# Performance work log

Measured on AMD Instinct MI355X. Metric: run time of the kernel, lower is better.

The kernel has to match this reference:

```python
import jax, jax.numpy as jnp
import numpy as np

B, S = 32, 128
VIDEO_SIZE, TITLE_SIZE = 768, 768
NUM_TAG, NUM_VOCAB, HIDDEN = 10000, 21128, 256


def setup_inputs() -> dict:
    key = jax.random.key(0)
    ks = jax.random.split(key, 10)
    video_feature = jax.random.normal(ks[0], (B, VIDEO_SIZE), dtype=jnp.float32)
    title_feature = jax.random.normal(ks[1], (B, S, TITLE_SIZE), dtype=jnp.float32)
    label_tag = jax.random.uniform(ks[2], (B, NUM_TAG), dtype=jnp.float32)
    label_mlm = jax.random.randint(ks[3], (B, S), 0, NUM_VOCAB, dtype=jnp.int64)
    Wt = jax.random.normal(ks[4], (NUM_TAG, VIDEO_SIZE), dtype=jnp.float32) * 0.02
    bt = jnp.zeros((NUM_TAG,), dtype=jnp.float32)
    Wm = jax.random.normal(ks[5], (NUM_VOCAB, TITLE_SIZE), dtype=jnp.float32) * 0.02
    bm = jnp.zeros((NUM_VOCAB,), dtype=jnp.float32)
    Wh = jax.random.normal(ks[6], (HIDDEN, VIDEO_SIZE + TITLE_SIZE), dtype=jnp.float32) * 0.02
    bh = jnp.zeros((HIDDEN,), dtype=jnp.float32)
    return {
        "video_feature": video_feature,
        "title_feature": title_feature,
        "label_tag": label_tag,
        "label_mlm": label_mlm,
        "Wt": Wt, "bt": bt, "Wm": Wm, "bm": bm, "Wh": Wh, "bh": bh,
    }


def reference(video_feature, title_feature, label_tag, label_mlm, Wt, bt, Wm, bm, Wh, bh):
    # tag head + BCEWithLogits (mean reduction), numerically stable form
    pred_tag = video_feature @ Wt.T + bt                       # [B, NUM_TAG]
    loss_tag = jnp.mean(
        jnp.maximum(pred_tag, 0.0) - pred_tag * label_tag
        + jnp.log1p(jnp.exp(-jnp.abs(pred_tag)))
    )
    pred_tag_sig = jax.nn.sigmoid(pred_tag)

    # mlm head: per-token vocab logits, masked CE summed over nonzero labels
    logits = jnp.einsum('bsd,vd->bsv', title_feature, Wm) + bm  # [B, S, V]
    lse = jax.nn.logsumexp(logits, axis=-1)                     # [B, S]
    gold = jnp.take_along_axis(logits, label_mlm[..., None], axis=-1)[..., 0]
    ce = lse - gold                                             # per-token NLL
    mask = (label_mlm != 0)
    loss_mlm = jnp.sum(jnp.where(mask, ce, 0.0))

    # fused embedding head + L2 normalize (torch eps 1e-12)
    feature = jnp.concatenate([video_feature, title_feature[:, 0]], axis=1)
    embedding = feature @ Wh.T + bh                             # [B, HIDDEN]
    norm = jnp.linalg.norm(embedding, axis=1, keepdims=True)
    normed_embedding = embedding / jnp.maximum(norm, 1e-12)

    return (pred_tag_sig, normed_embedding, loss_tag, loss_mlm)
```

## Files before the change

kernel.cpp:

```cpp
#include <hip/hip_runtime.h>
#include <hip/hip_bf16.h>
#include <math.h>

typedef short bf16x8 __attribute__((ext_vector_type(8)));
typedef float f32x4 __attribute__((ext_vector_type(4)));

#define KDIM 768
#define NTAG 10000
#define NVOC 21128
#define HID 256
#define NTOK 4096
#define NCHUNK 24
#define CHUNK 881
#define NTILE 28
#define TILEB 24576
#define M0 4.0f
#define WMSCALE 16.0f
#define INVSCALE 0.0625f
#define LOG2E 1.44269504f

#define WS_A     0ull
#define WS_AVID  3145728ull
#define WS_PSUM  3194880ull
#define WS_GOLD  3588096ull
#define WS_TAGL  3604480ull
#define WS_WM8   3604544ull
#define WS_NEED  (WS_WM8 + 16515072ull + 65536ull)

#define OUT_EMB  320000
#define OUT_LTAG 328192
#define OUT_LMLM 328193

#define MLM_BLKS 768
#define TAG_BLKS 313
#define GOLD_BLKS 256
#define EMB_BLKS 32
#define CONV_BLKS 1548
#define WMCV_BLKS (NCHUNK*NTILE)

typedef const __attribute__((address_space(1))) unsigned int glds_g;
typedef __attribute__((address_space(3))) unsigned int glds_l;

static __device__ __forceinline__ unsigned short f2bf(float f) {
  unsigned u = __builtin_bit_cast(unsigned, f);
  u = u + 0x7FFFu + ((u >> 16) & 1u);
  return (unsigned short)(u >> 16);
}

static __device__ __forceinline__ int pk4_fp8(float4 v, float scale) {
  int w = __builtin_amdgcn_cvt_pk_fp8_f32(v.x * scale, v.y * scale, 0, false);
  w = __builtin_amdgcn_cvt_pk_fp8_f32(v.z * scale, v.w * scale, w, true);
  return w;
}

static __device__ __forceinline__ bf16x8 cvt8(float4 f0, float4 f1) {
  bf16x8 o;
  o[0] = (short)f2bf(f0.x); o[1] = (short)f2bf(f0.y);
  o[2] = (short)f2bf(f0.z); o[3] = (short)f2bf(f0.w);
  o[4] = (short)f2bf(f1.x); o[5] = (short)f2bf(f1.y);
  o[6] = (short)f2bf(f1.z); o[7] = (short)f2bf(f1.w);
  return o;
}

__global__ __launch_bounds__(256) void k_conv(
    const float* __restrict__ title, const float* __restrict__ video,
    const float* __restrict__ Wm,
    char* __restrict__ A8, unsigned short* __restrict__ Avid,
    char* __restrict__ Wm8, float* __restrict__ tagSum) {
  __shared__ __align__(1024) char tsm[TILEB];
  const int bid = blockIdx.x, tid = threadIdx.x;
  if (bid < CONV_BLKS) {
    const int nT = 393216;
    int i = bid * 256 + tid;
    if (i == 0) tagSum[0] = 0.f;
    if (i < nT) {
      float4 v0 = ((const float4*)title)[i * 2];
      float4 v1 = ((const float4*)title)[i * 2 + 1];
      int2 o = {pk4_fp8(v0, 1.f), pk4_fp8(v1, 1.f)};
      *(int2*)(A8 + (size_t)i * 8) = o;
    } else {
      int j = i - nT;
      float4 v0 = ((const float4*)video)[j * 2];
      float4 v1 = ((const float4*)video)[j * 2 + 1];
      *(bf16x8*)(Avid + (size_t)j * 8) = cvt8(v0, v1);
    }
  } else {
    const int wblk = bid - CONV_BLKS;
    const int chunk = wblk / NTILE, tile = wblk % NTILE;
    const int n0 = chunk * CHUNK + tile * 32;
    const int nend = min(chunk * CHUNK + CHUNK, NVOC);
    #pragma unroll
    for (int j = 0; j < 12; ++j) {
      int p = j * 256 + tid;
      int r = p / 96, q = p % 96;
      int n = n0 + r;
      int2 o = {0, 0};
      if (n < nend) {
        const float* wp = Wm + (size_t)n * KDIM + q * 8;
        o.x = pk4_fp8(((const float4*)wp)[0], WMSCALE);
        o.y = pk4_fp8(((const float4*)wp)[1], WMSCALE);
      }
      *(int2*)(tsm + (q >> 2) * 1024 + (q & 3) * 256 + r * 8) = o;
    }
    __syncthreads();
    char* dst = Wm8 + (size_t)wblk * TILEB;
    #pragma unroll
    for (int j = 0; j < 6; ++j) {
      int idx = j * 256 + tid;
      *(int4*)(dst + idx * 16) = *(const int4*)(tsm + idx * 16);
    }
  }
}

template<bool WM8>
__global__ __launch_bounds__(256)
__attribute__((amdgpu_waves_per_eu(3, 3)))
void k_main(
    const char* __restrict__ A8,
    const float* __restrict__ Wm,
    const char* __restrict__ Wm8,
    const float* __restrict__ bm,
    float* __restrict__ psum,
    const unsigned short* __restrict__ Avid,
    const float* __restrict__ Wt, const float* __restrict__ bt,
    const float* __restrict__ ylab,
    const float* __restrict__ title, const int* __restrict__ lab,
    const float* __restrict__ video,
    const float* __restrict__ Wh, const float* __restrict__ bh,
    float* __restrict__ out_sig, float* __restrict__ tagSum,
    float* __restrict__ gold, float* __restrict__ out_emb) {
  __shared__ __align__(1024) char smem[2 * TILEB + 3584];
  const int bid = blockIdx.x, tid = threadIdx.x;
  const int wave = tid >> 6, lane = tid & 63, g = lane >> 4, col16 = lane & 15;

  if (bid < MLM_BLKS) {
    char (*Bsm)[TILEB] = (char(*)[TILEB])smem;
    float* biasS = (float*)(smem + 2 * TILEB);
    const int chunk = bid % NCHUNK, mt = bid / NCHUNK;
    const int nbeg = chunk * CHUNK;
    const int nend = min(nbeg + CHUNK, NVOC);
    const int col = col16;

    for (int i = tid; i < NTILE * 32; i += 256) {
      int n = nbeg + i;
      biasS[i] = (n < nend) ? (bm[n] - M0) * LOG2E : -1e30f;
    }

    const int arow0 = mt * 128 + wave * 32;
    long a0[24], a1[24];
    #pragma unroll
    for (int kk = 0; kk < 24; ++kk) {
      a0[kk] = *(const long*)(A8 + (size_t)(arow0 + col) * KDIM + kk * 32 + g * 8);
      a1[kk] = *(const long*)(A8 + (size_t)(arow0 + 16 + col) * KDIM + kk * 32 + g * 8);
    }

    float s[8];
    #pragma unroll
    for (int i = 0; i < 8; ++i) s[i] = 0.f;

    const int off0 = col * 8 + g * 256;
    const float kinv = INVSCALE * LOG2E;

    auto COMPUTE = [&](int t) {
      const char* B = &Bsm[t & 1][0] + off0;
      f32x4 acc00 = {0.f,0.f,0.f,0.f}, acc10 = {0.f,0.f,0.f,0.f};
      f32x4 acc01 = {0.f,0.f,0.f,0.f}, acc11 = {0.f,0.f,0.f,0.f};
      #pragma unroll
      for (int kk = 0; kk < 24; ++kk) {
        long b0 = *(const long*)(B + kk * 1024);
        long b1 = *(const long*)(B + kk * 1024 + 128);
        acc00 = __builtin_amdgcn_mfma_f32_16x16x32_fp8_fp8(a0[kk], b0, acc00, 0, 0, 0);
        acc10 = __builtin_amdgcn_mfma_f32_16x16x32_fp8_fp8(a1[kk], b0, acc10, 0, 0, 0);
        acc01 = __builtin_amdgcn_mfma_f32_16x16x32_fp8_fp8(a0[kk], b1, acc01, 0, 0, 0);
        acc11 = __builtin_amdgcn_mfma_f32_16x16x32_fp8_fp8(a1[kk], b1, acc11, 0, 0, 0);
      }
      const float b20 = biasS[t * 32 + col];
      const float b21 = biasS[t * 32 + 16 + col];
      #pragma unroll
      for (int rr = 0; rr < 4; ++rr) {
        s[rr]     += exp2f(fmaf(acc00[rr], kinv, b20)) + exp2f(fmaf(acc01[rr], kinv, b21));
        s[rr + 4] += exp2f(fmaf(acc10[rr], kinv, b20)) + exp2f(fmaf(acc11[rr], kinv, b21));
      }
    };

    if constexpr (WM8) {
      const char* cbase = Wm8 + (size_t)chunk * NTILE * TILEB;
      auto STAGE = [&](int buf, int tt) {
        const char* src = cbase + (size_t)tt * TILEB + wave * 1024 + lane * 16;
        char* dst = &Bsm[buf][0] + wave * 1024;
        #pragma unroll
        for (int j = 0; j < 6; ++j) {
          __builtin_amdgcn_global_load_lds((glds_g*)(src + j * 4096),
                                           (glds_l*)(dst + j * 4096), 16, 0, 0);
        }
      };
      STAGE(0, 0);
      asm volatile("s_waitcnt lgkmcnt(0)" ::: "memory");
      __builtin_amdgcn_s_barrier();
      for (int t = 0; t < NTILE; ++t) {
        int tn = (t + 1 < NTILE) ? t + 1 : 0;
        STAGE((t + 1) & 1, tn);
        asm volatile("s_waitcnt vmcnt(6)" ::: "memory");
        __builtin_amdgcn_s_barrier();
        __builtin_amdgcn_sched_barrier(0);
        __builtin_amdgcn_s_setprio(1);
        COMPUTE(t);
        __builtin_amdgcn_s_setprio(0);
        __builtin_amdgcn_sched_barrier(0);
        __builtin_amdgcn_s_barrier();
      }
    } else {
      __syncthreads();
      for (int t = 0; t < NTILE; ++t) {
        #pragma unroll
        for (int j = 0; j < 6; ++j) {
          int sg = j * 256 + tid;
          int kk = sg >> 6, gg = (sg >> 4) & 3, nl0 = (sg & 15) * 2;
          int n_a = nbeg + t * 32 + nl0, n_b = n_a + 1;
          int4 o = {0, 0, 0, 0};
          if (n_a < nend) {
            const float* wp = Wm + (size_t)n_a * KDIM + kk * 32 + gg * 8;
            o.x = pk4_fp8(((const float4*)wp)[0], WMSCALE);
            o.y = pk4_fp8(((const float4*)wp)[1], WMSCALE);
          }
          if (n_b < nend) {
            const float* wp = Wm + (size_t)n_b * KDIM + kk * 32 + gg * 8;
            o.z = pk4_fp8(((const float4*)wp)[0], WMSCALE);
            o.w = pk4_fp8(((const float4*)wp)[1], WMSCALE);
          }
          *(int4*)(&Bsm[0][0] + kk * 1024 + gg * 256 + nl0 * 8) = o;
        }
        __syncthreads();
        COMPUTE(t);
        __syncthreads();
      }
    }

    #pragma unroll
    for (int i = 0; i < 8; ++i) {
      float v = s[i];
      v += __shfl_xor(v, 1);
      v += __shfl_xor(v, 2);
      v += __shfl_xor(v, 4);
      v += __shfl_xor(v, 8);
      s[i] = v;
    }
    if (col == 0) {
      #pragma unroll
      for (int mblk = 0; mblk < 2; ++mblk)
        #pragma unroll
        for (int rr = 0; rr < 4; ++rr) {
          int tok = arow0 + mblk * 16 + g * 4 + rr;
          psum[tok * NCHUNK + chunk] = s[mblk * 4 + rr];
        }
    }

  } else if (bid < MLM_BLKS + TAG_BLKS) {
    const int tb = bid - MLM_BLKS;
    unsigned short* Bt = (unsigned short*)smem;
    float* wsum = (float*)(smem + 49152);
    #pragma unroll
    for (int j = 0; j < 12; ++j) {
      int sg = j * 256 + tid;
      int tt = (j >= 6) ? 1 : 0;
      int sgl = sg - tt * 1536;
      int kk = sgl >> 6, c = (sgl & 63) >> 2, gg = sgl & 3;
      int n = (tb * 2 + tt) * 16 + c;
      bf16x8 o = {};
      if (n < NTAG) {
        const float* wp = Wt + (size_t)n * KDIM + kk * 32 + gg * 8;
        o = cvt8(((const float4*)wp)[0], ((const float4*)wp)[1]);
      }
      *(bf16x8*)((char*)Bt + sg * 16) = o;
    }
    __syncthreads();

    const int ntile = tb * 2 + (wave >> 1), mhalf = wave & 1;
    float lacc = 0.f;
    if (ntile < 625) {
      bf16x8 a[24];
      #pragma unroll
      for (int kk = 0; kk < 24; ++kk)
        a[kk] = *(const bf16x8*)(Avid + (size_t)(mhalf * 16 + col16) * KDIM + kk * 32 + g * 8);
      const char* Bb = (const char*)Bt + (wave >> 1) * 24576 + col16 * 64 + g * 16;
      f32x4 acc = {0.f, 0.f, 0.f, 0.f};
      #pragma unroll
      for (int kk = 0; kk < 24; ++kk) {
        bf16x8 b = *(const bf16x8*)(Bb + kk * 1024);
        acc = __builtin_amdgcn_mfma_f32_16x16x32_bf16(a[kk], b, acc, 0, 0, 0);
      }
      const int nc = ntile * 16 + col16;
      if (nc < NTAG) {
        const float bias = bt[nc];
        #pragma unroll
        for (int rr = 0; rr < 4; ++rr) {
          int brow = mhalf * 16 + g * 4 + rr;
          float x = acc[rr] + bias;
          out_sig[(size_t)brow * NTAG + nc] = 1.f / (1.f + __expf(-x));
          float y = ylab[(size_t)brow * NTAG + nc];
          lacc += fmaxf(x, 0.f) - x * y + log1pf(__expf(-fabsf(x)));
        }
      }
    }
    #pragma unroll
    for (int m = 32; m; m >>= 1) lacc += __shfl_xor(lacc, m);
    if (lane == 0) wsum[wave] = lacc;
    __syncthreads();
    if (tid == 0) atomicAdd(tagSum, wsum[0] + wsum[1] + wsum[2] + wsum[3]);

  } else if (bid < MLM_BLKS + TAG_BLKS + GOLD_BLKS) {
    const int tbase = (bid - MLM_BLKS - TAG_BLKS) * 16;
    #pragma unroll
    for (int u = 0; u < 4; ++u) {
      int tok = tbase + wave * 4 + u;
      int l = lab[tok];
      float acc = 0.f;
      #pragma unroll
      for (int j = 0; j < 12; ++j) {
        int k = j * 64 + lane;
        acc += title[(size_t)tok * KDIM + k] * Wm[(size_t)l * KDIM + k];
      }
      #pragma unroll
      for (int m = 32; m; m >>= 1) acc += __shfl_xor(acc, m);
      if (lane == 0) gold[tok] = acc + bm[l];
    }

  } else {
    float* feat = (float*)smem;
    float* red = (float*)(smem + 49152);
    const int b = bid - MLM_BLKS - TAG_BLKS - GOLD_BLKS;
    #pragma unroll
    for (int j = 0; j < 6; ++j) {
      int k = j * 256 + tid;
      feat[k] = (k < KDIM) ? video[(size_t)b * KDIM + k]
                           : title[(size_t)b * 128 * KDIM + (k - KDIM)];
    }
    __syncthreads();
    float acc = bh[tid];
    #pragma unroll 8
    for (int k = 0; k < 1536; k += 4) {
      float4 w = *(const float4*)(Wh + (size_t)tid * 1536 + k);
      acc += w.x * feat[k] + w.y * feat[k + 1] + w.z * feat[k + 2] + w.w * feat[k + 3];
    }
    float ss = acc * acc;
    #pragma unroll
    for (int m = 32; m; m >>= 1) ss += __shfl_xor(ss, m);
    if (lane == 0) red[wave] = ss;
    __syncthreads();
    float nrm = sqrtf(red[0] + red[1] + red[2] + red[3]);
    float scale = 1.f / fmaxf(nrm, 1e-12f);
    out_emb[(size_t)b * HID + tid] = acc * scale;
  }
}

__global__ __launch_bounds__(256) void k_final(
    const float* __restrict__ psum, const float* __restrict__ gold,
    const int* __restrict__ lab, const float* __restrict__ tagSum,
    float* __restrict__ out) {
  __shared__ float red[4];
  const int tid = threadIdx.x, wave = tid >> 6, lane = tid & 63;
  if (tid == 0) out[OUT_LTAG] = tagSum[0] / 320000.f;

  float lm = 0.f;
  for (int tok = tid; tok < NTOK; tok += 256) {
    float S = 0.f;
    #pragma unroll
    for (int c = 0; c < NCHUNK; ++c) S += psum[tok * NCHUNK + c];
    float lse = M0 + logf(S);
    if (lab[tok] != 0) lm += lse - gold[tok];
  }
  #pragma unroll
  for (int m = 32; m; m >>= 1) lm += __shfl_xor(lm, m);
  if (lane == 0) red[wave] = lm;
  __syncthreads();
  if (tid == 0) out[OUT_LMLM] = red[0] + red[1] + red[2] + red[3];
}

extern "C" void kernel_launch(void* const* d_in, const int* in_sizes, int n_in,
                              void* d_out, int out_size, void* d_ws, size_t ws_size,
                              hipStream_t stream) {
  const float* video = (const float*)d_in[0];
  const float* title = (const float*)d_in[1];
  const float* ylab  = (const float*)d_in[2];
  const int*   lab   = (const int*)d_in[3];
  const float* Wt = (const float*)d_in[4];
  const float* bt = (const float*)d_in[5];
  const float* Wm = (const float*)d_in[6];
  const float* bm = (const float*)d_in[7];
  const float* Wh = (const float*)d_in[8];
  const float* bh = (const float*)d_in[9];
  float* out = (float*)d_out;
  char* ws = (char*)d_ws;

  char* wsA8   = ws + WS_A;
  unsigned short* wsAvid = (unsigned short*)(ws + WS_AVID);
  float* wsPsum = (float*)(ws + WS_PSUM);
  float* wsGold = (float*)(ws + WS_GOLD);
  float* wsTagl = (float*)(ws + WS_TAGL);
  char* wsWm8  = ws + WS_WM8;

  const bool useWm8 = ws_size >= WS_NEED;
  const int mainGrid = MLM_BLKS + TAG_BLKS + GOLD_BLKS + EMB_BLKS;

  k_conv<<<CONV_BLKS + WMCV_BLKS, 256, 0, stream>>>(
      title, video, Wm, wsA8, wsAvid, wsWm8, wsTagl);
  if (useWm8)
    k_main<true><<<mainGrid, 256, 0, stream>>>(
        wsA8, Wm, wsWm8, bm, wsPsum, wsAvid, Wt, bt, ylab, title, lab,
        video, Wh, bh, out, wsTagl, wsGold, out + OUT_EMB);
  else
    k_main<false><<<mainGrid, 256, 0, stream>>>(
        wsA8, Wm, wsWm8, bm, wsPsum, wsAvid, Wt, bt, ylab, title, lab,
        video, Wh, bh, out, wsTagl, wsGold, out + OUT_EMB);
  k_final<<<1, 256, 0, stream>>>(wsPsum, wsGold, lab, wsTagl, out);
}
```

Measured before the change: 161.6 us.

## Split fused main kernel into separate MLM and tail kernels

Splits the heterogeneous k_main kernel into k_mlm, which runs only the fp8 vocab GEMM blocks, and k_tail, which runs the tag, gold and embedding blocks. The tail kernel uses a small shared buffer and no forced waves-per-EU, and its tag path now reads Wt rows straight into registers instead of staging them in LDS, with a per-wave atomic in place of the block reduction. The aim is to stop the light blocks inheriting the large LDS footprint and register limits of the MLM blocks. The cost is an extra kernel launch, the loss of overlap between the tail work and the MLM GEMM, and more atomics on tagSum.

Result: slower. 197.4 us (+22.2%).

```diff
diff --git a/kernel.cpp b/kernel.cpp
--- a/kernel.cpp
+++ b/kernel.cpp
@@ -35,6 +35,7 @@
 #define TAG_BLKS 313
 #define GOLD_BLKS 256
 #define EMB_BLKS 32
+#define TAIL_GRID (TAG_BLKS + GOLD_BLKS + EMB_BLKS)
 #define CONV_BLKS 1548
 #define WMCV_BLKS (NCHUNK*NTILE)
 
@@ -115,201 +116,187 @@
 template<bool WM8>
 __global__ __launch_bounds__(256)
 __attribute__((amdgpu_waves_per_eu(3, 3)))
-void k_main(
+void k_mlm(
     const char* __restrict__ A8,
     const float* __restrict__ Wm,
     const char* __restrict__ Wm8,
     const float* __restrict__ bm,
-    float* __restrict__ psum,
+    float* __restrict__ psum) {
+  __shared__ __align__(1024) char smem[2 * TILEB + 3584];
+  char (*Bsm)[TILEB] = (char(*)[TILEB])smem;
+  float* biasS = (float*)(smem + 2 * TILEB);
+  const int tid = threadIdx.x;
+  const int wave = tid >> 6, lane = tid & 63, g = lane >> 4, col = lane & 15;
+  const int chunk = blockIdx.x % NCHUNK, mt = blockIdx.x / NCHUNK;
+  const int nbeg = chunk * CHUNK;
+  const int nend = min(nbeg + CHUNK, NVOC);
+
+  for (int i = tid; i < NTILE * 32; i += 256) {
+    int n = nbeg + i;
+    biasS[i] = (n < nend) ? (bm[n] - M0) * LOG2E : -1e30f;
+  }
+
+  const int arow0 = mt * 128 + wave * 32;
+  long a0[24], a1[24];
+  #pragma unroll
+  for (int kk = 0; kk < 24; ++kk) {
+    a0[kk] = *(const long*)(A8 + (size_t)(arow0 + col) * KDIM + kk * 32 + g * 8);
+    a1[kk] = *(const long*)(A8 + (size_t)(arow0 + 16 + col) * KDIM + kk * 32 + g * 8);
+  }
+
+  float s[8];
+  #pragma unroll
+  for (int i = 0; i < 8; ++i) s[i] = 0.f;
+
+  const int off0 = col * 8 + g * 256;
+  const float kinv = INVSCALE * LOG2E;
+
+  auto COMPUTE = [&](int t) {
+    const char* B = &Bsm[t & 1][0] + off0;
+    f32x4 acc00 = {0.f,0.f,0.f,0.f}, acc10 = {0.f,0.f,0.f,0.f};
+    f32x4 acc01 = {0.f,0.f,0.f,0.f}, acc11 = {0.f,0.f,0.f,0.f};
+    #pragma unroll
+    for (int kk = 0; kk < 24; ++kk) {
+      long b0 = *(const long*)(B + kk * 1024);
+      long b1 = *(const long*)(B + kk * 1024 + 128);
+      acc00 = __builtin_amdgcn_mfma_f32_16x16x32_fp8_fp8(a0[kk], b0, acc00, 0, 0, 0);
+      acc10 = __builtin_amdgcn_mfma_f32_16x16x32_fp8_fp8(a1[kk], b0, acc10, 0, 0, 0);
+      acc01 = __builtin_amdgcn_mfma_f32_16x16x32_fp8_fp8(a0[kk], b1, acc01, 0, 0, 0);
+      acc11 = __builtin_amdgcn_mfma_f32_16x16x32_fp8_fp8(a1[kk], b1, acc11, 0, 0, 0);
+    }
+    const float b20 = biasS[t * 32 + col];
+    const float b21 = biasS[t * 32 + 16 + col];
+    #pragma unroll
+    for (int rr = 0; rr < 4; ++rr) {
+      s[rr]     += exp2f(fmaf(acc00[rr], kinv, b20)) + exp2f(fmaf(acc01[rr], kinv, b21));
+      s[rr + 4] += exp2f(fmaf(acc10[rr], kinv, b20)) + exp2f(fmaf(acc11[rr], kinv, b21));
+    }
+  };
+
+  if constexpr (WM8) {
+    const char* cbase = Wm8 + (size_t)chunk * NTILE * TILEB;
+    auto STAGE = [&](int buf, int tt) {
+      const char* src = cbase + (size_t)tt * TILEB + wave * 1024 + lane * 16;
+      char* dst = &Bsm[buf][0] + wave * 1024;
+      #pragma unroll
+      for (int j = 0; j < 6; ++j) {
+        __builtin_amdgcn_global_load_lds((glds_g*)(src + j * 4096),
+                                         (glds_l*)(dst + j * 4096), 16, 0, 0);
+      }
+    };
+    STAGE(0, 0);
+    asm volatile("s_waitcnt lgkmcnt(0)" ::: "memory");
+    __builtin_amdgcn_s_barrier();
+    for (int t = 0; t < NTILE; ++t) {
+      int tn = (t + 1 < NTILE) ? t + 1 : 0;
+      STAGE((t + 1) & 1, tn);
+      asm volatile("s_waitcnt vmcnt(6)" ::: "memory");
+      __builtin_amdgcn_s_barrier();
+      __builtin_amdgcn_sched_barrier(0);
+      __builtin_amdgcn_s_setprio(1);
+      COMPUTE(t);
+      __builtin_amdgcn_s_setprio(0);
+      __builtin_amdgcn_sched_barrier(0);
+      __builtin_amdgcn_s_barrier();
+    }
+  } else {
+    __syncthreads();
+    for (int t = 0; t < NTILE; ++t) {
+      #pragma unroll
+      for (int j = 0; j < 6; ++j) {
+        int sg = j * 256 + tid;
+        int kk = sg >> 6, gg = (sg >> 4) & 3, nl0 = (sg & 15) * 2;
+        int n_a = nbeg + t * 32 + nl0, n_b = n_a + 1;
+        int4 o = {0, 0, 0, 0};
+        if (n_a < nend) {
+          const float* wp = Wm + (size_t)n_a * KDIM + kk * 32 + gg * 8;
+          o.x = pk4_fp8(((const float4*)wp)[0], WMSCALE);
+          o.y = pk4_fp8(((const float4*)wp)[1], WMSCALE);
+        }
+        if (n_b < nend) {
+          const float* wp = Wm + (size_t)n_b * KDIM + kk * 32 + gg * 8;
+          o.z = pk4_fp8(((const float4*)wp)[0], WMSCALE);
+          o.w = pk4_fp8(((const float4*)wp)[1], WMSCALE);
+        }
+        *(int4*)(&Bsm[0][0] + kk * 1024 + gg * 256 + nl0 * 8) = o;
+      }
+      __syncthreads();
+      COMPUTE(t);
+      __syncthreads();
+    }
+  }
+
+  #pragma unroll
+  for (int i = 0; i < 8; ++i) {
+    float v = s[i];
+    v += __shfl_xor(v, 1);
+    v += __shfl_xor(v, 2);
+    v += __shfl_xor(v, 4);
+    v += __shfl_xor(v, 8);
+    s[i] = v;
+  }
+  if (col == 0) {
+    #pragma unroll
+    for (int mblk = 0; mblk < 2; ++mblk)
+      #pragma unroll
+      for (int rr = 0; rr < 4; ++rr) {
+        int tok = arow0 + mblk * 16 + g * 4 + rr;
+        psum[tok * NCHUNK + chunk] = s[mblk * 4 + rr];
+      }
+  }
+}
+
+__global__ __launch_bounds__(256) void k_tail(
     const unsigned short* __restrict__ Avid,
+    const float* __restrict__ video, const float* __restrict__ title,
     const float* __restrict__ Wt, const float* __restrict__ bt,
-    const float* __restrict__ ylab,
-    const float* __restrict__ title, const int* __restrict__ lab,
-    const float* __restrict__ video,
+    const float* __restrict__ ylab, const int* __restrict__ lab,
+    const float* __restrict__ Wm, const float* __restrict__ bm,
     const float* __restrict__ Wh, const float* __restrict__ bh,
     float* __restrict__ out_sig, float* __restrict__ tagSum,
     float* __restrict__ gold, float* __restrict__ out_emb) {
-  __shared__ __align__(1024) char smem[2 * TILEB + 3584];
+  __shared__ __align__(64) float smem[1544];
   const int bid = blockIdx.x, tid = threadIdx.x;
-  const int wave = tid >> 6, lane = tid & 63, g = lane >> 4, col16 = lane & 15;
-
-  if (bid < MLM_BLKS) {
-    char (*Bsm)[TILEB] = (char(*)[TILEB])smem;
-    float* biasS = (float*)(smem + 2 * TILEB);
-    const int chunk = bid % NCHUNK, mt = bid / NCHUNK;
-    const int nbeg = chunk * CHUNK;
-    const int nend = min(nbeg + CHUNK, NVOC);
-    const int col = col16;
-
-    for (int i = tid; i < NTILE * 32; i += 256) {
-      int n = nbeg + i;
-      biasS[i] = (n < nend) ? (bm[n] - M0) * LOG2E : -1e30f;
-    }
-
-    const int arow0 = mt * 128 + wave * 32;
-    long a0[24], a1[24];
+  const int wave = tid >> 6, lane = tid & 63, g = lane >> 4, col = lane & 15;
+
+  if (bid < TAG_BLKS) {
+    const int unit = bid * 4 + wave;
+    if (unit >= 1250) return;
+    const int ntile = unit >> 1, mhalf = unit & 1;
+    const int n0 = ntile * 16;
+
+    bf16x8 a[24];
+    #pragma unroll
+    for (int kk = 0; kk < 24; ++kk)
+      a[kk] = *(const bf16x8*)(Avid + (size_t)(mhalf * 16 + col) * KDIM + kk * 32 + g * 8);
+
+    f32x4 acc = {0.f, 0.f, 0.f, 0.f};
+    const float* wrow = Wt + (size_t)(n0 + col) * KDIM;
     #pragma unroll
     for (int kk = 0; kk < 24; ++kk) {
-      a0[kk] = *(const long*)(A8 + (size_t)(arow0 + col) * KDIM + kk * 32 + g * 8);
-      a1[kk] = *(const long*)(A8 + (size_t)(arow0 + 16 + col) * KDIM + kk * 32 + g * 8);
-    }
-
-    float s[8];
-    #pragma unroll
-    for (int i = 0; i < 8; ++i) s[i] = 0.f;
-
-    const int off0 = col * 8 + g * 256;
-    const float kinv = INVSCALE * LOG2E;
-
-    auto COMPUTE = [&](int t) {
-      const char* B = &Bsm[t & 1][0] + off0;
-      f32x4 acc00 = {0.f,0.f,0.f,0.f}, acc10 = {0.f,0.f,0.f,0.f};
-      f32x4 acc01 = {0.f,0.f,0.f,0.f}, acc11 = {0.f,0.f,0.f,0.f};
-      #pragma unroll
-      for (int kk = 0; kk < 24; ++kk) {
-        long b0 = *(const long*)(B + kk * 1024);
-        long b1 = *(const long*)(B + kk * 1024 + 128);
-        acc00 = __builtin_amdgcn_mfma_f32_16x16x32_fp8_fp8(a0[kk], b0, acc00, 0, 0, 0);
-        acc10 = __builtin_amdgcn_mfma_f32_16x16x32_fp8_fp8(a1[kk], b0, acc10, 0, 0, 0);
-        acc01 = __builtin_amdgcn_mfma_f32_16x16x32_fp8_fp8(a0[kk], b1, acc01, 0, 0, 0);
-        acc11 = __builtin_amdgcn_mfma_f32_16x16x32_fp8_fp8(a1[kk], b1, acc11, 0, 0, 0);
-      }
-      const float b20 = biasS[t * 32 + col];
-      const float b21 = biasS[t * 32 + 16 + col];
-      #pragma unroll
-      for (int rr = 0; rr < 4; ++rr) {
-        s[rr]     += exp2f(fmaf(acc00[rr], kinv, b20)) + exp2f(fmaf(acc01[rr], kinv, b21));
-        s[rr + 4] += exp2f(fmaf(acc10[rr], kinv, b20)) + exp2f(fmaf(acc11[rr], kinv, b21));
-      }
-    };
-
-    if constexpr (WM8) {
-      const char* cbase = Wm8 + (size_t)chunk * NTILE * TILEB;
-      auto STAGE = [&](int buf, int tt) {
-        const char* src = cbase + (size_t)tt * TILEB + wave * 1024 + lane * 16;
-        char* dst = &Bsm[buf][0] + wave * 1024;
-        #pragma unroll
-        for (int j = 0; j < 6; ++j) {
-          __builtin_amdgcn_global_load_lds((glds_g*)(src + j * 4096),
-                                           (glds_l*)(dst + j * 4096), 16, 0, 0);
-        }
-      };
-      STAGE(0, 0);
-      asm volatile("s_waitcnt lgkmcnt(0)" ::: "memory");
-      __builtin_amdgcn_s_barrier();
-      for (int t = 0; t < NTILE; ++t) {
-        int tn = (t + 1 < NTILE) ? t + 1 : 0;
-        STAGE((t + 1) & 1, tn);
-        asm volatile("s_waitcnt vmcnt(6)" ::: "memory");
-        __builtin_amdgcn_s_barrier();
-        __builtin_amdgcn_sched_barrier(0);
-        __builtin_amdgcn_s_setprio(1);
-        COMPUTE(t);
-        __builtin_amdgcn_s_setprio(0);
-        __builtin_amdgcn_sched_barrier(0);
-        __builtin_amdgcn_s_barrier();
-      }
-    } else {
-      __syncthreads();
-      for (int t = 0; t < NTILE; ++t) {
-        #pragma unroll
-        for (int j = 0; j < 6; ++j) {
-          int sg = j * 256 + tid;
-          int kk = sg >> 6, gg = (sg >> 4) & 3, nl0 = (sg & 15) * 2;
-          int n_a = nbeg + t * 32 + nl0, n_b = n_a + 1;
-          int4 o = {0, 0, 0, 0};
-          if (n_a < nend) {
-            const float* wp = Wm + (size_t)n_a * KDIM + kk * 32 + gg * 8;
-            o.x = pk4_fp8(((const float4*)wp)[0], WMSCALE);
-            o.y = pk4_fp8(((const float4*)wp)[1], WMSCALE);
-          }
-          if (n_b < nend) {
-            const float* wp = Wm + (size_t)n_b * KDIM + kk * 32 + gg * 8;
-            o.z = pk4_fp8(((const float4*)wp)[0], WMSCALE);
-            o.w = pk4_fp8(((const float4*)wp)[1], WMSCALE);
-          }
-          *(int4*)(&Bsm[0][0] + kk * 1024 + gg * 256 + nl0 * 8) = o;
-        }
-        __syncthreads();
-        COMPUTE(t);
-        __syncthreads();
-      }
-    }
-
-    #pragma unroll
-    for (int i = 0; i < 8; ++i) {
-      float v = s[i];
-      v += __shfl_xor(v, 1);
-      v += __shfl_xor(v, 2);
-      v += __shfl_xor(v, 4);
-      v += __shfl_xor(v, 8);
-      s[i] = v;
-    }
-    if (col == 0) {
-      #pragma unroll
-      for (int mblk = 0; mblk < 2; ++mblk)
-        #pragma unroll
-        for (int rr = 0; rr < 4; ++rr) {
-          int tok = arow0 + mblk * 16 + g * 4 + rr;
-          psum[tok * NCHUNK + chunk] = s[mblk * 4 + rr];
-        }
-    }
-
-  } else if (bid < MLM_BLKS + TAG_BLKS) {
-    const int tb = bid - MLM_BLKS;
-    unsigned short* Bt = (unsigned short*)smem;
-    float* wsum = (float*)(smem + 49152);
-    #pragma unroll
-    for (int j = 0; j < 12; ++j) {
-      int sg = j * 256 + tid;
-      int tt = (j >= 6) ? 1 : 0;
-      int sgl = sg - tt * 1536;
-      int kk = sgl >> 6, c = (sgl & 63) >> 2, gg = sgl & 3;
-      int n = (tb * 2 + tt) * 16 + c;
-      bf16x8 o = {};
-      if (n < NTAG) {
-        const float* wp = Wt + (size_t)n * KDIM + kk * 32 + gg * 8;
-        o = cvt8(((const float4*)wp)[0], ((const float4*)wp)[1]);
-      }
-      *(bf16x8*)((char*)Bt + sg * 16) = o;
-    }
-    __syncthreads();
-
-    const int ntile = tb * 2 + (wave >> 1), mhalf = wave & 1;
+      float4 w0 = *(const float4*)(wrow + kk * 32 + g * 8);
+      float4 w1 = *(const float4*)(wrow + kk * 32 + g * 8 + 4);
+      bf16x8 b = cvt8(w0, w1);
+      acc = __builtin_amdgcn_mfma_f32_16x16x32_bf16(a[kk], b, acc, 0, 0, 0);
+    }
+
+    const int nc = n0 + col;
+    const float bias = bt[nc];
     float lacc = 0.f;
-    if (ntile < 625) {
-      bf16x8 a[24];
-      #pragma unroll
-      for (int kk = 0; kk < 24; ++kk)
-        a[kk] = *(const bf16x8*)(Avid + (size_t)(mhalf * 16 + col16) * KDIM + kk * 32 + g * 8);
-      const char* Bb = (const char*)Bt + (wave >> 1) * 24576 + col16 * 64 + g * 16;
-      f32x4 acc = {0.f, 0.f, 0.f, 0.f};
-      #pragma unroll
-      for (int kk = 0; kk < 24; ++kk) {
-        bf16x8 b = *(const bf16x8*)(Bb + kk * 1024);
-        acc = __builtin_amdgcn_mfma_f32_16x16x32_bf16(a[kk], b, acc, 0, 0, 0);
-      }
-      const int nc = ntile * 16 + col16;
-      if (nc < NTAG) {
-        const float bias = bt[nc];
-        #pragma unroll
-        for (int rr = 0; rr < 4; ++rr) {
-          int brow = mhalf * 16 + g * 4 + rr;
-          float x = acc[rr] + bias;
-          out_sig[(size_t)brow * NTAG + nc] = 1.f / (1.f + __expf(-x));
-          float y = ylab[(size_t)brow * NTAG + nc];
-          lacc += fmaxf(x, 0.f) - x * y + log1pf(__expf(-fabsf(x)));
-        }
-      }
+    #pragma unroll
+    for (int rr = 0; rr < 4; ++rr) {
+      int brow = mhalf * 16 + g * 4 + rr;
+      float x = acc[rr] + bias;
+      out_sig[(size_t)brow * NTAG + nc] = 1.f / (1.f + __expf(-x));
+      float y = ylab[(size_t)brow * NTAG + nc];
+      lacc += fmaxf(x, 0.f) - x * y + log1pf(__expf(-fabsf(x)));
     }
     #pragma unroll
     for (int m = 32; m; m >>= 1) lacc += __shfl_xor(lacc, m);
-    if (lane == 0) wsum[wave] = lacc;
-    __syncthreads();
-    if (tid == 0) atomicAdd(tagSum, wsum[0] + wsum[1] + wsum[2] + wsum[3]);
-
-  } else if (bid < MLM_BLKS + TAG_BLKS + GOLD_BLKS) {
-    const int tbase = (bid - MLM_BLKS - TAG_BLKS) * 16;
+    if (lane == 0) atomicAdd(tagSum, lacc);
+
+  } else if (bid < TAG_BLKS + GOLD_BLKS) {
+    const int tbase = (bid - TAG_BLKS) * 16;
     #pragma unroll
     for (int u = 0; u < 4; ++u) {
       int tok = tbase + wave * 4 + u;
@@ -326,9 +313,9 @@
     }
 
   } else {
-    float* feat = (float*)smem;
-    float* red = (float*)(smem + 49152);
-    const int b = bid - MLM_BLKS - TAG_BLKS - GOLD_BLKS;
+    float* feat = smem;
+    float* red = smem + 1536;
+    const int b = bid - TAG_BLKS - GOLD_BLKS;
     #pragma unroll
     for (int j = 0; j < 6; ++j) {
       int k = j * 256 + tid;
@@ -400,17 +387,15 @@
   char* wsWm8  = ws + WS_WM8;
 
   const bool useWm8 = ws_size >= WS_NEED;
-  const int mainGrid = MLM_BLKS + TAG_BLKS + GOLD_BLKS + EMB_BLKS;
 
   k_conv<<<CONV_BLKS + WMCV_BLKS, 256, 0, stream>>>(
       title, video, Wm, wsA8, wsAvid, wsWm8, wsTagl);
   if (useWm8)
-    k_main<true><<<mainGrid, 256, 0, stream>>>(
-        wsA8, Wm, wsWm8, bm, wsPsum, wsAvid, Wt, bt, ylab, title, lab,
-        video, Wh, bh, out, wsTagl, wsGold, out + OUT_EMB);
+    k_mlm<true><<<MLM_BLKS, 256, 0, stream>>>(wsA8, Wm, wsWm8, bm, wsPsum);
   else
-    k_main<false><<<mainGrid, 256, 0, stream>>>(
-        wsA8, Wm, wsWm8, bm, wsPsum, wsAvid, Wt, bt, ylab, title, lab,
-        video, Wh, bh, out, wsTagl, wsGold, out + OUT_EMB);
+    k_mlm<false><<<MLM_BLKS, 256, 0, stream>>>(wsA8, Wm, wsWm8, bm, wsPsum);
+  k_tail<<<TAIL_GRID, 256, 0, stream>>>(
+      wsAvid, video, title, Wt, bt, ylab, lab, Wm, bm, Wh, bh,
+      out, wsTagl, wsGold, out + OUT_EMB);
   k_final<<<1, 256, 0, stream>>>(wsPsum, wsGold, lab, wsTagl, out);
 }
```
